# Kernel optimization log

Measured on AMD Instinct MI355X. Metric: run time of the kernel, lower is better.

## Reference

```python
import jax, jax.numpy as jnp
import numpy as np

B, C, N = 32, 1024, 512
OUTDIM = 256
EPS_SQRT = 1e-12   # clamp before sqrt so diagonal zeros stay differentiable
EPS_NORM = 1e-12   # torch F.normalize eps


def setup_inputs() -> dict:
    key = jax.random.key(0)
    k1, k2, k3, k4, k5 = jax.random.split(key, 5)
    xi = jax.random.normal(k1, (B, 256, N), dtype=jnp.float32)
    xh = jax.random.normal(k2, (B, 256, N), dtype=jnp.float32)
    xo = jax.random.normal(k3, (B, C, N), dtype=jnp.float32)
    # LazyLinear(outdim) materializes as Linear(N*N, outdim)
    fan_in = N * N
    bound = 1.0 / np.sqrt(fan_in)
    W = jax.random.uniform(k4, (fan_in, OUTDIM), dtype=jnp.float32, minval=-bound, maxval=bound)
    b = jax.random.uniform(k5, (OUTDIM,), dtype=jnp.float32, minval=-bound, maxval=bound)
    return {"xi": xi, "xh": xh, "xo": xo, "W": W, "b": b}


def reference(xi, xh, xo, W, b):
    # xi, xh are unused by SoGA.forward
    x = jnp.transpose(xo, (0, 2, 1))                 # [B, N, C]
    # similarity (Gram) matrix over points
    S = jnp.einsum('bnc,bmc->bnm', x, x)             # [B, N, N], symmetric
    # pairwise Euclidean distance between rows of S
    sq = jnp.sum(S * S, axis=-1)                     # [B, N]
    G = jnp.einsum('bnk,bmk->bnm', S, S)             # [B, N, N]
    d2 = sq[:, :, None] + sq[:, None, :] - 2.0 * G
    D = jnp.sqrt(jnp.maximum(d2, EPS_SQRT))          # [B, N, N]
    flat = D.reshape(D.shape[0], -1)                 # [B, N*N]
    d_out = flat @ W + b                             # [B, outdim]
    norm = jnp.maximum(jnp.linalg.norm(d_out, axis=-1, keepdims=True), EPS_NORM)
    return d_out / norm
```

## Files before the change

kernel.cpp:

```cpp
#include <hip/hip_runtime.h>

typedef unsigned short ushort_t;
typedef __attribute__((ext_vector_type(8))) unsigned short ushort8;
typedef __attribute__((ext_vector_type(4))) unsigned short ushort4v;
typedef __attribute__((ext_vector_type(8))) __bf16 bf16x8;
typedef __attribute__((ext_vector_type(4))) float f32x4;
typedef __attribute__((ext_vector_type(4))) float f4;
typedef __attribute__((ext_vector_type(4))) unsigned int uint4v;

#define B_ 32
#define C_ 1024
#define N_ 512
#define O_ 256

__device__ inline float bf2f(unsigned short u) {
  unsigned int i = ((unsigned int)u) << 16;
  return __builtin_bit_cast(float, i);
}
__device__ inline unsigned short f2bf(float f) {
  unsigned int i = __builtin_bit_cast(unsigned int, f);
  i += 0x7FFFu + ((i >> 16) & 1u);
  return (unsigned short)(i >> 16);
}

#define DOT2(acc_, a_, b_)                                                  \
  asm("v_dot2_f32_bf16 %0, %1, %2, %0" : "+v"(acc_) : "v"(a_), "v"(b_))
#define CVTPK(dst_, lo_, hi_)                                               \
  asm("v_cvt_pk_bf16_f32 %0, %1, %2" : "=v"(dst_) : "v"(lo_), "v"(hi_))

__device__ inline void gl_lds16(const ushort_t* g, ushort_t* l) {
  __builtin_amdgcn_global_load_lds(
      (const __attribute__((address_space(1))) void*)g,
      (__attribute__((address_space(3))) void*)l, 16, 0, 0);
}

__global__ __launch_bounds__(256) void k_transpose(const float* __restrict__ xo,
                                                   ushort_t* __restrict__ xoT) {
  __shared__ float tile[64][65];
  const int tn = blockIdx.x, tc = blockIdx.y, b = blockIdx.z;
  const int c0 = tc * 64, n0 = tn * 64;
  const int t = threadIdx.x;
  const int tr = t >> 4, tq = t & 15;
  const float* src = xo + ((size_t)b * C_ + c0) * N_ + n0;
#pragma unroll
  for (int p = 0; p < 4; ++p) {
    int c = p * 16 + tr;
    f4 v = *(const f4*)(src + (size_t)c * N_ + tq * 4);
    tile[c][tq * 4 + 0] = v[0];
    tile[c][tq * 4 + 1] = v[1];
    tile[c][tq * 4 + 2] = v[2];
    tile[c][tq * 4 + 3] = v[3];
  }
  __syncthreads();
  ushort_t* dst = xoT + ((size_t)b * N_ + n0) * C_ + c0;
#pragma unroll
  for (int p = 0; p < 4; ++p) {
    int n = p * 16 + tr;
    ushort4v u;
#pragma unroll
    for (int j = 0; j < 4; ++j) u[j] = f2bf(tile[tq * 4 + j][n]);
    *(ushort4v*)(dst + (size_t)n * C_ + tq * 4) = u;
  }
}

template <int KSTEPS, int LDK>
__device__ inline void gemm_main(const ushort_t* __restrict__ Arows,
                                 const ushort_t* __restrict__ Brows,
                                 ushort_t* lds, f32x4 (&acc)[4][4], int t) {
  ushort_t* lds_a = lds;
  ushort_t* lds_b = lds + 8192;
  const int lane = t & 63, w = t >> 6;
  const int wr = w >> 1, wc = w & 1;
  const int l16 = lane & 15, lg = lane >> 4;
  const int srow = w * 32 + (lane >> 2);
  const int skp = (((lane & 3) ^ ((lane >> 3) & 3)) * 8);
  const int lgsw = ((lg ^ ((l16 >> 1) & 3))) * 8;
#define STAGE(s_, buf_)                                                     \
  {                                                                         \
    _Pragma("unroll") for (int j = 0; j < 2; ++j) {                         \
      const int row = srow + j * 16;                                        \
      gl_lds16(Arows + (size_t)row * LDK + (s_)*32 + skp,                   \
               lds_a + (buf_)*4096 + (w * 2 + j) * 512);                    \
      gl_lds16(Brows + (size_t)row * LDK + (s_)*32 + skp,                   \
               lds_b + (buf_)*4096 + (w * 2 + j) * 512);                    \
    }                                                                       \
  }
  STAGE(0, 0)
  __syncthreads();
  int buf = 0;
  for (int s = 0; s < KSTEPS; ++s) {
    if (s + 1 < KSTEPS) STAGE(s + 1, buf ^ 1)
    ushort8 au[4], bu[4];
#pragma unroll
    for (int i = 0; i < 4; ++i) {
      au[i] = *(const ushort8*)&lds_a[buf * 4096 + (wr * 64 + i * 16 + l16) * 32 + lgsw];
      bu[i] = *(const ushort8*)&lds_b[buf * 4096 + (wc * 64 + i * 16 + l16) * 32 + lgsw];
    }
#pragma unroll
    for (int ai = 0; ai < 4; ++ai)
#pragma unroll
      for (int bi = 0; bi < 4; ++bi)
        acc[ai][bi] = __builtin_amdgcn_mfma_f32_16x16x32_bf16(
            __builtin_bit_cast(bf16x8, au[ai]), __builtin_bit_cast(bf16x8, bu[bi]),
            acc[ai][bi], 0, 0, 0);
    __syncthreads();
    buf ^= 1;
  }
#undef STAGE
}

#define CT_LD 136

__global__ __launch_bounds__(256, 3) void k_sgemm(const ushort_t* __restrict__ xoT,
                                                  ushort_t* __restrict__ S,
                                                  float* __restrict__ sqp) {
  __shared__ ushort_t lds[128 * CT_LD];
  const int b = blockIdx.y, tile = blockIdx.x;
  const int n0 = (tile >> 2) * 128, m0 = (tile & 3) * 128;
  const int mt = tile & 3;
  const ushort_t* Ab = xoT + (size_t)b * N_ * C_ + (size_t)n0 * C_;
  const ushort_t* Bb = xoT + (size_t)b * N_ * C_ + (size_t)m0 * C_;
  f32x4 acc[4][4] = {};
  const int t = threadIdx.x;
  gemm_main<C_ / 32, C_>(Ab, Bb, lds, acc, t);
  const int lane = t & 63, w = t >> 6, wr = w >> 1, wc = w & 1;
  const int l16 = lane & 15, lg = lane >> 4;
#pragma unroll
  for (int ai = 0; ai < 4; ++ai)
#pragma unroll
    for (int bi = 0; bi < 4; ++bi)
#pragma unroll
      for (int j = 0; j < 4; ++j) {
        int r = wr * 64 + ai * 16 + lg * 4 + j;
        int c = wc * 64 + bi * 16 + l16;
        lds[r * CT_LD + c] = f2bf(acc[ai][bi][j]);
      }
  __syncthreads();
  ushort_t* Sb = S + (size_t)b * N_ * N_;
  float* sqpb = sqp + ((size_t)mt * B_ + b) * N_ + n0;
#pragma unroll
  for (int p = 0; p < 8; ++p) {
    int id = p * 256 + t;
    int r = id >> 4, cc = (id & 15) * 8;
    ushort8 v = *(const ushort8*)&lds[r * CT_LD + cc];
    *(ushort8*)(Sb + (size_t)(n0 + r) * N_ + m0 + cc) = v;
    float s8 = 0.f;
#pragma unroll
    for (int j = 0; j < 8; ++j) {
      float f = bf2f(v[j]);
      s8 += f * f;
    }
    s8 += __shfl_xor(s8, 1, 64);
    s8 += __shfl_xor(s8, 2, 64);
    s8 += __shfl_xor(s8, 4, 64);
    s8 += __shfl_xor(s8, 8, 64);
    if ((t & 15) == 0) sqpb[r] = s8;
  }
}

__global__ __launch_bounds__(256, 3) void k_dgemm(const ushort_t* __restrict__ S,
                                                  const float* __restrict__ sqp,
                                                  ushort_t* __restrict__ D) {
  __shared__ ushort_t lds[128 * CT_LD];
  __shared__ float sqn[128], sqm[128];
  const int b = blockIdx.y, tile = blockIdx.x;
  const int n0 = (tile >> 2) * 128, m0 = (tile & 3) * 128;
  const int t = threadIdx.x;
  {
    const int idx = (t < 128) ? (n0 + t) : (m0 + (t - 128));
    float s = 0.f;
#pragma unroll
    for (int mt = 0; mt < 4; ++mt) s += sqp[((size_t)mt * B_ + b) * N_ + idx];
    if (t < 128)
      sqn[t] = s;
    else
      sqm[t - 128] = s;
  }
  const ushort_t* Ab = S + (size_t)b * N_ * N_ + (size_t)n0 * N_;
  const ushort_t* Bb = S + (size_t)b * N_ * N_ + (size_t)m0 * N_;
  f32x4 acc[4][4] = {};
  gemm_main<N_ / 32, N_>(Ab, Bb, lds, acc, t);
  const int lane = t & 63, w = t >> 6, wr = w >> 1, wc = w & 1;
  const int l16 = lane & 15, lg = lane >> 4;
#pragma unroll
  for (int ai = 0; ai < 4; ++ai)
#pragma unroll
    for (int bi = 0; bi < 4; ++bi)
#pragma unroll
      for (int j = 0; j < 4; ++j) {
        int nl = wr * 64 + ai * 16 + lg * 4 + j;
        int ml = wc * 64 + bi * 16 + l16;
        float d2 = sqn[nl] + sqm[ml] - 2.f * acc[ai][bi][j];
        lds[nl * CT_LD + ml] = f2bf(sqrtf(fmaxf(d2, 1e-12f)));
      }
  __syncthreads();
  ushort_t* Db = D + (size_t)b * N_ * N_;
#pragma unroll
  for (int p = 0; p < 8; ++p) {
    int id = p * 256 + t;
    int r = id >> 4, cc = (id & 15) * 8;
    *(ushort8*)(Db + (size_t)(n0 + r) * N_ + m0 + cc) = *(const ushort8*)&lds[r * CT_LD + cc];
  }
}

__global__ __launch_bounds__(256, 2) void k_dw(const ushort_t* __restrict__ Dm,
                                               const float* __restrict__ W,
                                               float* __restrict__ partial) {
  __shared__ ushort_t lds_d[32 * 512];
  const int g = blockIdx.x, t = threadIdx.x;
  const int k0 = g * 512;
  const int w = t >> 6, lane = t & 63;
#pragma unroll
  for (int i = 0; i < 8; ++i) {
    int c = i * 256 + t;
    gl_lds16(Dm + (size_t)(c >> 6) * (N_ * N_) + k0 + (c & 63) * 8,
             lds_d + (i * 256 + w * 64) * 8);
  }
  __syncthreads();
  const int ks = w;
  const int ob = lane * 4;
  float acc[32][4] = {};
  const float* Wb = W + ((size_t)(k0 + ks * 128)) * O_ + ob;
  const ushort_t* dbase = &lds_d[ks * 128];
  f4 rA[8], rB[8];
  unsigned int wp[4][4];
#define LOADRAW(dst, kb_)                                                    \
  {                                                                          \
    _Pragma("unroll") for (int r = 0; r < 8; ++r) dst[r] =                   \
        *(const f4*)(Wb + (size_t)((kb_)*8 + r) * O_);                       \
  }
#define CVT(raw_)                                                            \
  {                                                                          \
    _Pragma("unroll") for (int r = 0; r < 4; ++r) {                          \
      CVTPK(wp[r][0], raw_[2 * r][0], raw_[2 * r + 1][0]);                   \
      CVTPK(wp[r][1], raw_[2 * r][1], raw_[2 * r + 1][1]);                   \
      CVTPK(wp[r][2], raw_[2 * r][2], raw_[2 * r + 1][2]);                   \
      CVTPK(wp[r][3], raw_[2 * r][3], raw_[2 * r + 1][3]);                   \
    }                                                                        \
  }
#define COMP(kb_)                                                            \
  {                                                                          \
    const int kl = (kb_)*8;                                                  \
    _Pragma("unroll") for (int bb = 0; bb < 32; ++bb) {                      \
      uint4v dv4 = *(const uint4v*)&dbase[bb * 512 + kl];                    \
      _Pragma("unroll") for (int j = 0; j < 4; ++j) {                        \
        DOT2(acc[bb][0], dv4[j], wp[j][0]);                                  \
        DOT2(acc[bb][1], dv4[j], wp[j][1]);                                  \
        DOT2(acc[bb][2], dv4[j], wp[j][2]);                                  \
        DOT2(acc[bb][3], dv4[j], wp[j][3]);                                  \
      }                                                                      \
    }                                                                        \
  }
  LOADRAW(rA, 0)
#pragma unroll 1
  for (int kb = 0; kb < 16; kb += 2) {
    LOADRAW(rB, kb + 1)
    CVT(rA)
    COMP(kb)
    if (kb + 2 < 16) LOADRAW(rA, kb + 2)
    CVT(rB)
    COMP(kb + 1)
  }
#undef LOADRAW
#undef CVT
#undef COMP
  __syncthreads();
  float* lds_f = (float*)lds_d;
#pragma unroll
  for (int c = 0; c < 4; ++c) {
#pragma unroll
    for (int q = 0; q < 8; ++q) {
      f4 v;
      v[0] = acc[c * 8 + q][0];
      v[1] = acc[c * 8 + q][1];
      v[2] = acc[c * 8 + q][2];
      v[3] = acc[c * 8 + q][3];
      *(f4*)&lds_f[(ks * 8 + q) * 256 + lane * 4] = v;
    }
    __syncthreads();
    {
      const int q2 = t >> 5, o = (t & 31) * 8;
      f4 s0 = {}, s1 = {};
#pragma unroll
      for (int k2 = 0; k2 < 4; ++k2) {
        f4 a0 = *(const f4*)&lds_f[(k2 * 8 + q2) * 256 + o];
        f4 a1 = *(const f4*)&lds_f[(k2 * 8 + q2) * 256 + o + 4];
        s0 += a0;
        s1 += a1;
      }
      float* P = partial + ((size_t)g * B_ + c * 8 + q2) * O_ + o;
      *(f4*)P = s0;
      *(f4*)(P + 4) = s1;
    }
    __syncthreads();
  }
}

__global__ __launch_bounds__(256) void k_red1(const float* __restrict__ partial,
                                              float* __restrict__ p2) {
  const int pg = blockIdx.x, b = blockIdx.y, t = threadIdx.x;
  float s = 0.f;
#pragma unroll 8
  for (int p = pg * 64; p < pg * 64 + 64; ++p)
    s += partial[((size_t)p * B_ + b) * O_ + t];
  p2[((size_t)pg * B_ + b) * O_ + t] = s;
}

__global__ __launch_bounds__(256) void k_red2(const float* __restrict__ p2,
                                              const float* __restrict__ bias,
                                              float* __restrict__ out) {
  const int b = blockIdx.x, t = threadIdx.x;
  float s = 0.f;
#pragma unroll
  for (int pg = 0; pg < 8; ++pg) s += p2[((size_t)pg * B_ + b) * O_ + t];
  s += bias[t];
  float q = s * s;
#pragma unroll
  for (int off = 32; off; off >>= 1) q += __shfl_down(q, off, 64);
  __shared__ float lds[4];
  if ((t & 63) == 0) lds[t >> 6] = q;
  __syncthreads();
  float tot = lds[0] + lds[1] + lds[2] + lds[3];
  out[b * O_ + t] = s / fmaxf(sqrtf(tot), 1e-12f);
}

extern "C" void kernel_launch(void* const* d_in, const int* in_sizes, int n_in,
                              void* d_out, int out_size, void* d_ws, size_t ws_size,
                              hipStream_t stream) {
  const float* xo = (const float*)d_in[2];
  const float* W = (const float*)d_in[3];
  const float* bias = (const float*)d_in[4];
  float* out = (float*)d_out;

  char* ws = (char*)d_ws;
  const size_t OFF_S = 33554432, OFF_D = 50331648, OFF_SQP = 67108864,
               OFF_P2 = 67371008, NEED = 67633152;
  if (ws_size < NEED) return;
  ushort_t* xoT = (ushort_t*)ws;
  ushort_t* S = (ushort_t*)(ws + OFF_S);
  ushort_t* D = (ushort_t*)(ws + OFF_D);
  float* sqp = (float*)(ws + OFF_SQP);
  float* p2 = (float*)(ws + OFF_P2);
  float* partial = (float*)ws;

  hipLaunchKernelGGL(k_transpose, dim3(8, 16, 32), dim3(256), 0, stream, xo, xoT);
  hipLaunchKernelGGL(k_sgemm, dim3(16, 32), dim3(256), 0, stream, xoT, S, sqp);
  hipLaunchKernelGGL(k_dgemm, dim3(16, 32), dim3(256), 0, stream, S, sqp, D);
  hipLaunchKernelGGL(k_dw, dim3(512), dim3(256), 0, stream, D, W, partial);
  hipLaunchKernelGGL(k_red1, dim3(8, 32), dim3(256), 0, stream, partial, p2);
  hipLaunchKernelGGL(k_red2, dim3(32), dim3(256), 0, stream, p2, bias, out);
}
```

Before: 147.5 us.

## Exploit Gram symmetry: compute only upper-triangular tiles in S and D GEMMs

Both the S=XXᵀ and G=SSᵀ GEMMs now launch only the 10 upper-triangular 128x128 tiles per batch instead of all 16. Off-diagonal tiles also write their transpose through strided LDS reads, and the transposed block's row sum-of-squares partials are emitted too. This cuts MFMA work by roughly 37.5% in the two dominant GEMMs. In exchange it adds strided, bank-conflict-prone LDS transpose reads, extra stores in off-diagonal blocks, and a less even grid of 320 blocks.

```diff
diff --git a/kernel.cpp b/kernel.cpp
--- a/kernel.cpp
+++ b/kernel.cpp
@@ -33,6 +33,9 @@
       (const __attribute__((address_space(1))) void*)g,
       (__attribute__((address_space(3))) void*)l, 16, 0, 0);
 }
+
+__device__ __constant__ const int TRI_NT[10] = {0, 0, 0, 0, 1, 1, 1, 2, 2, 3};
+__device__ __constant__ const int TRI_MT[10] = {0, 1, 2, 3, 1, 2, 3, 2, 3, 3};
 
 __global__ __launch_bounds__(256) void k_transpose(const float* __restrict__ xo,
                                                    ushort_t* __restrict__ xoT) {
@@ -115,9 +118,9 @@
                                                   ushort_t* __restrict__ S,
                                                   float* __restrict__ sqp) {
   __shared__ ushort_t lds[128 * CT_LD];
-  const int b = blockIdx.y, tile = blockIdx.x;
-  const int n0 = (tile >> 2) * 128, m0 = (tile & 3) * 128;
-  const int mt = tile & 3;
+  const int b = blockIdx.x, y = blockIdx.y;
+  const int nt = TRI_NT[y], mt = TRI_MT[y];
+  const int n0 = nt * 128, m0 = mt * 128;
   const ushort_t* Ab = xoT + (size_t)b * N_ * C_ + (size_t)n0 * C_;
   const ushort_t* Bb = xoT + (size_t)b * N_ * C_ + (size_t)m0 * C_;
   f32x4 acc[4][4] = {};
@@ -137,24 +140,49 @@
       }
   __syncthreads();
   ushort_t* Sb = S + (size_t)b * N_ * N_;
-  float* sqpb = sqp + ((size_t)mt * B_ + b) * N_ + n0;
-#pragma unroll
-  for (int p = 0; p < 8; ++p) {
-    int id = p * 256 + t;
-    int r = id >> 4, cc = (id & 15) * 8;
-    ushort8 v = *(const ushort8*)&lds[r * CT_LD + cc];
-    *(ushort8*)(Sb + (size_t)(n0 + r) * N_ + m0 + cc) = v;
-    float s8 = 0.f;
-#pragma unroll
-    for (int j = 0; j < 8; ++j) {
-      float f = bf2f(v[j]);
-      s8 += f * f;
-    }
-    s8 += __shfl_xor(s8, 1, 64);
-    s8 += __shfl_xor(s8, 2, 64);
-    s8 += __shfl_xor(s8, 4, 64);
-    s8 += __shfl_xor(s8, 8, 64);
-    if ((t & 15) == 0) sqpb[r] = s8;
+  {
+    float* sqpb = sqp + ((size_t)mt * B_ + b) * N_ + n0;
+#pragma unroll
+    for (int p = 0; p < 8; ++p) {
+      int id = p * 256 + t;
+      int r = id >> 4, cc = (id & 15) * 8;
+      ushort8 v = *(const ushort8*)&lds[r * CT_LD + cc];
+      *(ushort8*)(Sb + (size_t)(n0 + r) * N_ + m0 + cc) = v;
+      float s8 = 0.f;
+#pragma unroll
+      for (int j = 0; j < 8; ++j) {
+        float f = bf2f(v[j]);
+        s8 += f * f;
+      }
+      s8 += __shfl_xor(s8, 1, 64);
+      s8 += __shfl_xor(s8, 2, 64);
+      s8 += __shfl_xor(s8, 4, 64);
+      s8 += __shfl_xor(s8, 8, 64);
+      if ((t & 15) == 0) sqpb[r] = s8;
+    }
+  }
+  if (nt != mt) {
+    float* sqpc = sqp + ((size_t)nt * B_ + b) * N_ + m0;
+#pragma unroll
+    for (int p = 0; p < 8; ++p) {
+      int id = p * 256 + t;
+      int rr = id >> 4, cc = (id & 15) * 8;
+      ushort8 v;
+#pragma unroll
+      for (int j = 0; j < 8; ++j) v[j] = lds[(cc + j) * CT_LD + rr];
+      *(ushort8*)(Sb + (size_t)(m0 + rr) * N_ + n0 + cc) = v;
+      float s8 = 0.f;
+#pragma unroll
+      for (int j = 0; j < 8; ++j) {
+        float f = bf2f(v[j]);
+        s8 += f * f;
+      }
+      s8 += __shfl_xor(s8, 1, 64);
+      s8 += __shfl_xor(s8, 2, 64);
+      s8 += __shfl_xor(s8, 4, 64);
+      s8 += __shfl_xor(s8, 8, 64);
+      if ((t & 15) == 0) sqpc[rr] = s8;
+    }
   }
 }
 
@@ -163,14 +191,15 @@
                                                   ushort_t* __restrict__ D) {
   __shared__ ushort_t lds[128 * CT_LD];
   __shared__ float sqn[128], sqm[128];
-  const int b = blockIdx.y, tile = blockIdx.x;
-  const int n0 = (tile >> 2) * 128, m0 = (tile & 3) * 128;
+  const int b = blockIdx.x, y = blockIdx.y;
+  const int nt = TRI_NT[y], mt = TRI_MT[y];
+  const int n0 = nt * 128, m0 = mt * 128;
   const int t = threadIdx.x;
   {
     const int idx = (t < 128) ? (n0 + t) : (m0 + (t - 128));
     float s = 0.f;
 #pragma unroll
-    for (int mt = 0; mt < 4; ++mt) s += sqp[((size_t)mt * B_ + b) * N_ + idx];
+    for (int p = 0; p < 4; ++p) s += sqp[((size_t)p * B_ + b) * N_ + idx];
     if (t < 128)
       sqn[t] = s;
     else
@@ -200,6 +229,17 @@
     int id = p * 256 + t;
     int r = id >> 4, cc = (id & 15) * 8;
     *(ushort8*)(Db + (size_t)(n0 + r) * N_ + m0 + cc) = *(const ushort8*)&lds[r * CT_LD + cc];
+  }
+  if (nt != mt) {
+#pragma unroll
+    for (int p = 0; p < 8; ++p) {
+      int id = p * 256 + t;
+      int rr = id >> 4, cc = (id & 15) * 8;
+      ushort8 v;
+#pragma unroll
+      for (int j = 0; j < 8; ++j) v[j] = lds[(cc + j) * CT_LD + rr];
+      *(ushort8*)(Db + (size_t)(m0 + rr) * N_ + n0 + cc) = v;
+    }
   }
 }
 
@@ -344,8 +384,8 @@
   float* partial = (float*)ws;
 
   hipLaunchKernelGGL(k_transpose, dim3(8, 16, 32), dim3(256), 0, stream, xo, xoT);
-  hipLaunchKernelGGL(k_sgemm, dim3(16, 32), dim3(256), 0, stream, xoT, S, sqp);
-  hipLaunchKernelGGL(k_dgemm, dim3(16, 32), dim3(256), 0, stream, S, sqp, D);
+  hipLaunchKernelGGL(k_sgemm, dim3(32, 10), dim3(256), 0, stream, xoT, S, sqp);
+  hipLaunchKernelGGL(k_dgemm, dim3(32, 10), dim3(256), 0, stream, S, sqp, D);
   hipLaunchKernelGGL(k_dw, dim3(512), dim3(256), 0, stream, D, W, partial);
   hipLaunchKernelGGL(k_red1, dim3(8, 32), dim3(256), 0, stream, partial, p2);
   hipLaunchKernelGGL(k_red2, dim3(32), dim3(256), 0, stream, p2, bias, out);
```

Result: faster. 140.2 us (-4.9%).
